# Optimization experiments

Hardware: AMD Instinct MI355X
Metric: run time of the kernel (lower is better)

## Reference

```python
import jax, jax.numpy as jnp
import numpy as np

B, T = 8192, 4096

def setup_inputs() -> dict:
    key = jax.random.key(0)
    x = jax.random.randint(key, (B, T, 1), 0, 5).astype(jnp.float32)
    alpha = jnp.full((1, 1), 0.1, dtype=jnp.float32)  # smoothing weight for demand level Z
    beta = jnp.full((1, 1), 0.1, dtype=jnp.float32)   # smoothing weight for demand probability P
    return {"x": x, "alpha": alpha, "beta": beta}


def reference(x, alpha, beta):
    # Faithful translation of the Keras TSBRNN cell stepped over time by RNN().
    # NOTE (faithful to source): the cell unpacks states as (Z, P) but returns
    # them as [P_next, Z_next], so the two states SWAP roles every step.
    # Also faithful: X = inputs[0] uses only the FIRST batch row's value in the
    # level update, while the zero-mask is computed over the full batch.
    batch = x.shape[0]

    def step(carry, x_t):
        Z, P = carry                      # each (B, 1)
        X = x_t[0]                        # (1,) first batch row, as in source
        nz = (x_t != 0).astype(x_t.dtype) # (B, 1) non-zero demand mask
        Z_next = alpha * X + (1.0 - alpha) * Z
        Z_next = Z_next * nz + Z * (1.0 - nz)
        P_next = nz * beta + (1.0 - beta) * P
        out = P_next * Z_next             # TSB forecast = prob * level
        return (P_next, Z_next), out      # swapped order, faithful to source

    Z0 = jnp.zeros((batch, 1), x.dtype)
    P0 = jnp.zeros((batch, 1), x.dtype)
    xs = jnp.swapaxes(x, 0, 1)            # (T, B, 1) time-major for scan
    _, ys = jax.lax.scan(step, (Z0, P0), xs)
    return jnp.swapaxes(ys, 0, 1)         # (B, T, 1) full output sequence
```

## Files before the change

kernel.cpp:

```cpp
#include <hip/hip_runtime.h>


constexpr int T_LEN  = 4096;
constexpr int TILE   = 1024;
constexpr int NTILE  = T_LEN / TILE;
constexpr int CHUNK  = TILE / 64;
constexpr int WPB    = 4;
constexpr int PADREG = TILE + TILE / 16;

__global__ __launch_bounds__(256) void tsb_scan_kernel(
    const float* __restrict__ x,
    const float* __restrict__ alpha_p,
    const float* __restrict__ beta_p,
    float* __restrict__ out,
    int B)
{
    __shared__ float lds[WPB * PADREG];

    const int tid  = threadIdx.x;
    const int wave = tid >> 6;
    const int lane = tid & 63;
    const int row  = blockIdx.x * WPB + wave;
    if (row >= B) return;

    float* xl = &lds[wave * PADREG];

    const float a   = alpha_p[0];
    const float b   = beta_p[0];
    const float oma = 1.0f - a;
    const float omb = 1.0f - b;

    float C1 = 0.f, C2 = 0.f;

    for (int t = 0; t < NTILE; ++t) {
        const float4* xr4 = (const float4*)(x + (size_t)row * T_LEN + t * TILE);
        const float4* Xr4 = (const float4*)(x + t * TILE);

        float xs[16];
#pragma unroll
        for (int i = 0; i < 4; ++i)
            *(float4*)(xs + 4 * i) = xr4[i * 64 + lane];

        float Xc[CHUNK];
#pragma unroll
        for (int m = 0; m < 4; ++m)
            *(float4*)(Xc + 4 * m) = Xr4[4 * lane + m];

#pragma unroll
        for (int j = 0; j < 16; ++j) {
            int e  = (j >> 2) * 256 + 4 * lane + (j & 3);
            int ap = e + (e >> 4);
            xl[ap] = xs[j];
        }
        float xc[CHUNK];
        const int cb = 17 * lane;
#pragma unroll
        for (int j = 0; j < CHUNK; ++j)
            xc[j] = xl[cb + j];

        float p = 1.f, u = 0.f, q = 1.f, v = 0.f;
#pragma unroll
        for (int h = 0; h < CHUNK / 2; ++h) {
            float x1 = xc[2 * h], x2 = xc[2 * h + 1];
            float X1 = Xc[2 * h], X2 = Xc[2 * h + 1];
            float nz1 = (x1 != 0.f) ? 1.f : 0.f;
            float nz2 = (x2 != 0.f) ? 1.f : 0.f;
            float k1  = (x1 != 0.f) ? oma : 1.f;
            float k2  = (x2 != 0.f) ? oma : 1.f;
            float P = omb * k1;
            float U = omb * a * nz1 * X1 + b * nz2;
            float Q = omb * k2;
            float V = b * k2 * nz1 + a * nz2 * X2;
            u = P * u + U;  p = P * p;
            v = Q * v + V;  q = Q * q;
        }

#pragma unroll
        for (int off = 1; off < 64; off <<= 1) {
            float pi = __shfl_up(p, off, 64);
            float ui = __shfl_up(u, off, 64);
            float qi = __shfl_up(q, off, 64);
            float vi = __shfl_up(v, off, 64);
            if (lane >= off) {
                u = p * ui + u;  p = p * pi;
                v = q * vi + v;  q = q * qi;
            }
        }
        float pp = __shfl_up(p, 1, 64), up = __shfl_up(u, 1, 64);
        float qp = __shfl_up(q, 1, 64), vp = __shfl_up(v, 1, 64);
        float c1 = (lane == 0) ? C1 : (pp * C1 + up);
        float c2 = (lane == 0) ? C2 : (qp * C2 + vp);
        float p63 = __shfl(p, 63, 64), u63 = __shfl(u, 63, 64);
        float q63 = __shfl(q, 63, 64), v63 = __shfl(v, 63, 64);
        float C1n = p63 * C1 + u63;
        float C2n = q63 * C2 + v63;
        C1 = C1n;  C2 = C2n;

#pragma unroll
        for (int j = 0; j < CHUNK; ++j) {
            float xj = xc[j];
            bool  nz = (xj != 0.f);
            float c2n = nz ? (a * Xc[j] + oma * c1) : c1;
            float c1n = (nz ? b : 0.f) + omb * c2;
            c1 = c1n;  c2 = c2n;
            xl[cb + j] = c1 * c2;
        }

        float4* or4 = (float4*)(out + (size_t)row * T_LEN + t * TILE);
#pragma unroll
        for (int i = 0; i < 4; ++i) {
            float os[4];
#pragma unroll
            for (int k = 0; k < 4; ++k) {
                int e = i * 256 + 4 * lane + k;
                os[k] = xl[e + (e >> 4)];
            }
            or4[i * 64 + lane] = *(float4*)os;
        }
    }
}

extern "C" void kernel_launch(void* const* d_in, const int* in_sizes, int n_in,
                              void* d_out, int out_size, void* d_ws, size_t ws_size,
                              hipStream_t stream) {
    const float* x     = (const float*)d_in[0];
    const float* alpha = (const float*)d_in[1];
    const float* beta  = (const float*)d_in[2];
    float* out = (float*)d_out;

    const int B = in_sizes[0] / T_LEN;
    const int blocks = (B + WPB - 1) / WPB;
    tsb_scan_kernel<<<blocks, 64 * WPB, 0, stream>>>(x, alpha, beta, out, B);
}
```

Baseline: 237.7 us.

## Double-buffer row tiles via async global-to-LDS loads with XOR-swizzled layout

Replaces the register-staged global loads and padded LDS transpose with direct global_load_lds DMA into a per-wave double buffer, so the next tile is prefetched while the current tile is being scanned. The LDS layout now uses an XOR swizzle instead of padding, which allows float4 LDS reads and writes. Out-of-range waves are clamped to the last row instead of returning, because the DMA path needs every lane active. This relies on manual vmcnt waits and sched barriers, and the swizzle and wait count must match exactly.

```diff
diff --git a/kernel.cpp b/kernel.cpp
--- a/kernel.cpp
+++ b/kernel.cpp
@@ -1,12 +1,19 @@
 #include <hip/hip_runtime.h>
+#include <stdint.h>
 
 
-constexpr int T_LEN  = 4096;
-constexpr int TILE   = 1024;
-constexpr int NTILE  = T_LEN / TILE;
-constexpr int CHUNK  = TILE / 64;
-constexpr int WPB    = 4;
-constexpr int PADREG = TILE + TILE / 16;
+constexpr int T_LEN = 4096;
+constexpr int TILE  = 1024;
+constexpr int NTILE = T_LEN / TILE;
+constexpr int CHUNK = TILE / 64;
+constexpr int WPB   = 4;
+
+typedef const __attribute__((address_space(1))) uint32_t* gas_ptr;
+typedef __attribute__((address_space(3))) uint32_t* las_ptr;
+
+__device__ __forceinline__ void dma16(const float* g, float* l) {
+    __builtin_amdgcn_global_load_lds((gas_ptr)g, (las_ptr)l, 16, 0, 0);
+}
 
 __global__ __launch_bounds__(256) void tsb_scan_kernel(
     const float* __restrict__ x,
@@ -15,48 +22,60 @@
     float* __restrict__ out,
     int B)
 {
-    __shared__ float lds[WPB * PADREG];
+    __shared__ __align__(16) float lds[WPB * 2 * TILE];
 
     const int tid  = threadIdx.x;
     const int wave = tid >> 6;
     const int lane = tid & 63;
-    const int row  = blockIdx.x * WPB + wave;
-    if (row >= B) return;
+    int row = blockIdx.x * WPB + wave;
+    if (row >= B) row = B - 1;
 
-    float* xl = &lds[wave * PADREG];
+    float* const buf0 = &lds[wave * 2 * TILE];
 
     const float a   = alpha_p[0];
     const float b   = beta_p[0];
     const float oma = 1.0f - a;
     const float omb = 1.0f - b;
 
+    const int lam = lane ^ ((lane >> 3) & 7);
+    const float* xrow = x + (size_t)row * T_LEN;
+
+    {
+        const float* g = xrow + lam * 4;
+#pragma unroll
+        for (int i = 0; i < 4; ++i)
+            dma16(g + i * 256, buf0 + i * 256);
+    }
+
     float C1 = 0.f, C2 = 0.f;
 
+#pragma unroll
     for (int t = 0; t < NTILE; ++t) {
-        const float4* xr4 = (const float4*)(x + (size_t)row * T_LEN + t * TILE);
-        const float4* Xr4 = (const float4*)(x + t * TILE);
-
-        float xs[16];
-#pragma unroll
-        for (int i = 0; i < 4; ++i)
-            *(float4*)(xs + 4 * i) = xr4[i * 64 + lane];
+        float* const buf = buf0 + (t & 1) * TILE;
 
         float Xc[CHUNK];
+        const float4* Xr4 = (const float4*)(x + t * TILE);
 #pragma unroll
         for (int m = 0; m < 4; ++m)
             *(float4*)(Xc + 4 * m) = Xr4[4 * lane + m];
 
+        if (t < NTILE - 1) {
+            float* const nbuf = buf0 + ((t + 1) & 1) * TILE;
+            const float* g = xrow + (t + 1) * TILE + lam * 4;
 #pragma unroll
-        for (int j = 0; j < 16; ++j) {
-            int e  = (j >> 2) * 256 + 4 * lane + (j & 3);
-            int ap = e + (e >> 4);
-            xl[ap] = xs[j];
+            for (int i = 0; i < 4; ++i)
+                dma16(g + i * 256, nbuf + i * 256);
         }
+
+        asm volatile("s_waitcnt vmcnt(8)" ::: "memory");
+        __builtin_amdgcn_sched_barrier(0);
+
         float xc[CHUNK];
-        const int cb = 17 * lane;
 #pragma unroll
-        for (int j = 0; j < CHUNK; ++j)
-            xc[j] = xl[cb + j];
+        for (int j = 0; j < 4; ++j) {
+            int slot = (4 * lane + j) ^ ((lane >> 1) & 7);
+            *(float4*)(xc + 4 * j) = *(const float4*)&buf[slot * 4];
+        }
 
         float p = 1.f, u = 0.f, q = 1.f, v = 0.f;
 #pragma unroll
@@ -97,25 +116,31 @@
         C1 = C1n;  C2 = C2n;
 
 #pragma unroll
-        for (int j = 0; j < CHUNK; ++j) {
-            float xj = xc[j];
-            bool  nz = (xj != 0.f);
-            float c2n = nz ? (a * Xc[j] + oma * c1) : c1;
-            float c1n = (nz ? b : 0.f) + omb * c2;
-            c1 = c1n;  c2 = c2n;
-            xl[cb + j] = c1 * c2;
+        for (int j = 0; j < 4; ++j) {
+            float o[4];
+#pragma unroll
+            for (int k = 0; k < 2; ++k) {
+                int idx = 4 * j + 2 * k;
+                float xA = xc[idx], xB = xc[idx + 1];
+                bool  nzA = (xA != 0.f);
+                float c2A = nzA ? (a * Xc[idx] + oma * c1) : c1;
+                float c1A = (nzA ? b : 0.f) + omb * c2;
+                bool  nzB = (xB != 0.f);
+                float c2B = nzB ? (a * Xc[idx + 1] + oma * c1A) : c1A;
+                float c1B = (nzB ? b : 0.f) + omb * c2A;
+                c1 = c1B;  c2 = c2B;
+                o[2 * k]     = c1A * c2A;
+                o[2 * k + 1] = c1B * c2B;
+            }
+            int slot = (4 * lane + j) ^ ((lane >> 1) & 7);
+            *(float4*)&buf[slot * 4] = *(float4*)o;
         }
 
         float4* or4 = (float4*)(out + (size_t)row * T_LEN + t * TILE);
 #pragma unroll
         for (int i = 0; i < 4; ++i) {
-            float os[4];
-#pragma unroll
-            for (int k = 0; k < 4; ++k) {
-                int e = i * 256 + 4 * lane + k;
-                os[k] = xl[e + (e >> 4)];
-            }
-            or4[i * 64 + lane] = *(float4*)os;
+            int slot = i * 64 + lam;
+            or4[i * 64 + lane] = *(const float4*)&buf[slot * 4];
         }
     }
 }
```

New measurement: 234.5 us. Within noise of the previous version (-1.4%).
